# Kernel tuning notes

Measured on AMD Instinct MI355X. Metric: run time of the kernel, lower is better.

Reference implementation:

```python
import jax, jax.numpy as jnp
import numpy as np

GROUPS = 32
EPS = 1e-5
N_HEADS = 4


def group_norm(x, w, b):
    # x: [B, C, T]; GroupNorm over (C/G, T) within each of G groups
    B, C, T = x.shape
    xg = x.reshape(B, GROUPS, (C // GROUPS) * T)
    mean = xg.mean(axis=-1, keepdims=True)
    var = xg.var(axis=-1, keepdims=True)
    xn = ((xg - mean) * jax.lax.rsqrt(var + EPS)).reshape(B, C, T)
    return xn * w[None, :, None] + b[None, :, None]


def setup_inputs() -> dict:
    key = jax.random.key(0)
    ks = jax.random.split(key, 5)
    B, C, H, W = 2, 256, 64, 64
    x = jax.random.normal(ks[0], (B, C, H, W), dtype=jnp.float32)
    norm_w = jnp.ones((C,), dtype=jnp.float32)
    norm_b = jnp.zeros((C,), dtype=jnp.float32)
    qkv_w = jax.random.normal(ks[1], (3 * C, C), dtype=jnp.float32) * (C ** -0.5)
    qkv_b = jax.random.normal(ks[2], (3 * C,), dtype=jnp.float32) * 0.02
    proj_w = jax.random.normal(ks[3], (C, C), dtype=jnp.float32) * (C ** -0.5)
    proj_b = jax.random.normal(ks[4], (C,), dtype=jnp.float32) * 0.02
    return {"x": x, "norm_w": norm_w, "norm_b": norm_b,
            "qkv_w": qkv_w, "qkv_b": qkv_b,
            "proj_w": proj_w, "proj_b": proj_b}


def reference(x, norm_w, norm_b, qkv_w, qkv_b, proj_w, proj_b):
    B, C, Hs, Ws = x.shape
    T = Hs * Ws
    xf = x.reshape(B, C, T)
    xn = group_norm(xf, norm_w, norm_b)
    # 1x1 conv1d == channel matmul: [3C,C] x [B,C,T] -> [B,3C,T]
    qkv = jnp.einsum('oc,bct->bot', qkv_w, xn) + qkv_b[None, :, None]
    ch = C // N_HEADS
    # legacy order: [B, H*3*ch, T] -> [B*H, 3*ch, T] -> split
    qkv_h = qkv.reshape(B * N_HEADS, 3 * ch, T)
    q, k, v = qkv_h[:, :ch], qkv_h[:, ch:2 * ch], qkv_h[:, 2 * ch:]
    scale = ch ** -0.25
    # full [B*H, T, T] score matrix, softmax in fp32 (faithful to source)
    weight = jnp.einsum('bct,bcs->bts', q * scale, k * scale)
    weight = jax.nn.softmax(weight.astype(jnp.float32), axis=-1).astype(qkv.dtype)
    a = jnp.einsum('bts,bcs->bct', weight, v).reshape(B, C, T)
    h = jnp.einsum('oc,bct->bot', proj_w, a) + proj_b[None, :, None]
    return (xf + h).reshape(B, C, Hs, Ws)
```

## Files before the change

### kernel.cpp

```cpp
#include <hip/hip_runtime.h>
#include <hip/hip_bf16.h>

#define B_    2
#define C_    256
#define T_    4096
#define GRP   32
#define CPG   8
#define NH    4
#define CH    64
#define K3C   768
#define SPLIT 4
#define GSL   8
#define LOG2E 1.4426950408889634f

typedef __attribute__((ext_vector_type(8))) short bf16x8;
typedef __attribute__((ext_vector_type(4))) float f32x4;

#if __has_builtin(__builtin_amdgcn_exp2f)
#define EXP2(x) __builtin_amdgcn_exp2f(x)
#else
#define EXP2(x) exp2f(x)
#endif

__device__ __forceinline__ unsigned pk2(float a, float b) {
    __hip_bfloat162 h = __float22bfloat162_rn(make_float2(a, b));
    union { __hip_bfloat162 h2; unsigned u; } cv; cv.h2 = h;
    return cv.u;
}
__device__ __forceinline__ float bf2f(unsigned short u) {
    return __uint_as_float((unsigned)u << 16);
}

__global__ __launch_bounds__(256) void cvt_kernel(
    const float* __restrict__ qw, const float* __restrict__ pw,
    unsigned short* __restrict__ qwb, unsigned short* __restrict__ pwb) {
    int i = blockIdx.x * 256 + threadIdx.x;
    const int n1 = K3C * C_ / 8;
    const float* src; unsigned short* dst;
    if (i < n1) { src = qw + 8 * i; dst = qwb + 8 * i; }
    else { int j = i - n1; src = pw + 8 * j; dst = pwb + 8 * j; }
    float4 a = *(const float4*)src;
    float4 b = *(const float4*)(src + 4);
    uint4 u;
    u.x = pk2(a.x, a.y); u.y = pk2(a.z, a.w);
    u.z = pk2(b.x, b.y); u.w = pk2(b.z, b.w);
    *(uint4*)dst = u;
}

__global__ __launch_bounds__(256) void gn_stats_kernel(
    const float* __restrict__ x, float* __restrict__ stat) {
    int bg = blockIdx.x, sl = blockIdx.y;
    const int SLN = CPG * T_ / GSL;
    const float* xp = x + (size_t)bg * CPG * T_ + (size_t)sl * SLN;
    int tid = threadIdx.x;

    float s = 0.f, s2 = 0.f;
    for (int i = tid * 4; i < SLN; i += 1024) {
        float4 v = *(const float4*)&xp[i];
        s  += (v.x + v.y) + (v.z + v.w);
        s2 += (v.x * v.x + v.y * v.y) + (v.z * v.z + v.w * v.w);
    }
    for (int off = 32; off > 0; off >>= 1) {
        s  += __shfl_down(s,  off);
        s2 += __shfl_down(s2, off);
    }
    __shared__ float rs[4], rs2[4];
    int wid = tid >> 6;
    if ((tid & 63) == 0) { rs[wid] = s; rs2[wid] = s2; }
    __syncthreads();
    if (tid == 0) {
        float a = (rs[0] + rs[1]) + (rs[2] + rs[3]);
        float a2 = (rs2[0] + rs2[1]) + (rs2[2] + rs2[3]);
        stat[(bg * GSL + sl) * 2]     = a;
        stat[(bg * GSL + sl) * 2 + 1] = a2;
    }
}

__global__ __launch_bounds__(256) void gn_apply_kernel(
    const float* __restrict__ x, const float* __restrict__ stat,
    const float* __restrict__ w, const float* __restrict__ b,
    unsigned short* __restrict__ xnT) {
    int bg = blockIdx.x, sl = blockIdx.y;
    int batch = bg / GRP, g = bg % GRP;
    const float* xp = x + (size_t)bg * CPG * T_;
    int tid = threadIdx.x;

    float s = 0.f, s2 = 0.f;
#pragma unroll
    for (int i = 0; i < GSL; ++i) {
        s  += stat[(bg * GSL + i) * 2];
        s2 += stat[(bg * GSL + i) * 2 + 1];
    }
    float inv_n = 1.f / (float)(CPG * T_);
    float mean = s * inv_n;
    float var  = s2 * inv_n - mean * mean;
    float inv  = rsqrtf(var + 1e-5f);

    float wv[8], bv[8];
#pragma unroll
    for (int j = 0; j < 8; j++) {
        float ww = w[g * CPG + j] * inv;
        wv[j] = ww;
        bv[j] = b[g * CPG + j] - mean * ww;
    }
    unsigned short* op = xnT + (size_t)batch * T_ * C_ + g * CPG;
    int t0 = sl * (T_ / GSL);
#pragma unroll
    for (int rep = 0; rep < 2; ++rep) {
        int t = t0 + rep * 256 + tid;
        float v[8];
#pragma unroll
        for (int j = 0; j < 8; j++) v[j] = xp[(size_t)j * T_ + t] * wv[j] + bv[j];
        uint4 u;
        u.x = pk2(v[0], v[1]); u.y = pk2(v[2], v[3]);
        u.z = pk2(v[4], v[5]); u.w = pk2(v[6], v[7]);
        *(uint4*)&op[(size_t)t * C_] = u;
    }
}

__global__ __launch_bounds__(256) void qkv_gemm_kernel(
    const unsigned short* __restrict__ Wb, const float* __restrict__ bias,
    const unsigned short* __restrict__ Xt, unsigned short* __restrict__ q_t,
    unsigned short* __restrict__ k_t, unsigned short* __restrict__ v_d) {
    int tb = blockIdx.x * 128;
    int by = blockIdx.y;
    int bz = blockIdx.z;
    int ob = by * 64;
    int tid = threadIdx.x;
    int l = tid & 15, oct = (tid >> 4) & 3, w = tid >> 6;

    __shared__ __align__(16) unsigned short SH[64 * 264];

#pragma unroll
    for (int j = 0; j < 8; ++j) {
        int idx = tid + 256 * j;
        int row = idx >> 5, ch = idx & 31;
        *(uint4*)&SH[row * 264 + ch * 8] =
            *(const uint4*)&Wb[(size_t)(ob + row) * C_ + ch * 8];
    }
    __syncthreads();

    const unsigned short* Xb = Xt + (size_t)bz * T_ * C_;

    f32x4 acc[4][2];
#pragma unroll
    for (int mf = 0; mf < 4; ++mf)
#pragma unroll
        for (int nf = 0; nf < 2; ++nf) acc[mf][nf] = (f32x4){0.f, 0.f, 0.f, 0.f};

#pragma unroll
    for (int kk = 0; kk < 8; ++kk) {
        int c0 = 32 * kk + 8 * oct;
        bf16x8 bfr[2];
#pragma unroll
        for (int nf = 0; nf < 2; ++nf)
            bfr[nf] = *(const bf16x8*)&Xb[(size_t)(tb + 32 * w + 16 * nf + l) * C_ + c0];
#pragma unroll
        for (int mf = 0; mf < 4; ++mf) {
            bf16x8 af = *(const bf16x8*)&SH[(16 * mf + l) * 264 + c0];
#pragma unroll
            for (int nf = 0; nf < 2; ++nf)
                acc[mf][nf] = __builtin_amdgcn_mfma_f32_16x16x32_bf16(af, bfr[nf], acc[mf][nf], 0, 0, 0);
        }
    }

    int head = by / 3, sec = by - 3 * head;
    int bh = bz * NH + head;

    if (sec < 2) {
        float scale = (sec == 0) ? 0.125f * LOG2E : 1.f;
        unsigned short* dst = ((sec == 0) ? q_t : k_t) + (size_t)bh * T_ * CH;
#pragma unroll
        for (int mf = 0; mf < 4; ++mf) {
            float bvs[4];
#pragma unroll
            for (int r = 0; r < 4; ++r) bvs[r] = bias[ob + 16 * mf + 4 * oct + r];
#pragma unroll
            for (int nf = 0; nf < 2; ++nf) {
                int t = tb + 32 * w + 16 * nf + l;
                float v0 = (acc[mf][nf][0] + bvs[0]) * scale;
                float v1 = (acc[mf][nf][1] + bvs[1]) * scale;
                float v2 = (acc[mf][nf][2] + bvs[2]) * scale;
                float v3 = (acc[mf][nf][3] + bvs[3]) * scale;
                uint2 u; u.x = pk2(v0, v1); u.y = pk2(v2, v3);
                *(uint2*)&dst[(size_t)t * CH + 16 * mf + 4 * oct] = u;
            }
        }
    } else {
        __syncthreads();
#pragma unroll
        for (int mf = 0; mf < 4; ++mf) {
            float bvs[4];
#pragma unroll
            for (int r = 0; r < 4; ++r) bvs[r] = bias[ob + 16 * mf + 4 * oct + r];
#pragma unroll
            for (int nf = 0; nf < 2; ++nf) {
                int tl = 32 * w + 16 * nf + l;
#pragma unroll
                for (int r = 0; r < 4; ++r) {
                    unsigned pv = pk2(acc[mf][nf][r] + bvs[r], 0.f);
                    SH[(16 * mf + 4 * oct + r) * 136 + tl] = (unsigned short)(pv & 0xffffu);
                }
            }
        }
        __syncthreads();
        unsigned short* vdst = v_d + (size_t)bh * CH * T_;
#pragma unroll
        for (int j = 0; j < 4; ++j) {
            int idx = tid + 256 * j;
            int row = idx >> 4, ch = idx & 15;
            *(uint4*)&vdst[(size_t)row * T_ + tb + ch * 8] =
                *(uint4*)&SH[row * 136 + ch * 8];
        }
    }
}

__global__ __launch_bounds__(256, 4) void attn_kernel(
    const unsigned short* __restrict__ q_t, const unsigned short* __restrict__ k_t,
    const unsigned short* __restrict__ v_d, unsigned short* __restrict__ Opart,
    float* __restrict__ lbuf) {
    int bh = blockIdx.y;
    int sp = blockIdx.z;
    int t0 = blockIdx.x * 128;
    int tid = threadIdx.x;
    int l = tid & 15, q = (tid >> 4) & 3, w = tid >> 6;

    __shared__ __align__(16) unsigned short Kt[64][72];
    __shared__ __align__(16) unsigned short Vt[64][72];
    __shared__ __align__(16) unsigned short Ps[128][72];

    const unsigned short* qb = q_t + (size_t)bh * T_ * CH;
    const unsigned short* kb = k_t + (size_t)bh * T_ * CH;
    const unsigned short* vb = v_d + (size_t)bh * CH * T_;

    bf16x8 qf[2][2];
#pragma unroll
    for (int nf = 0; nf < 2; ++nf) {
        int t = t0 + 32 * w + 16 * nf + l;
#pragma unroll
        for (int kk = 0; kk < 2; ++kk)
            qf[nf][kk] = *(const bf16x8*)&qb[(size_t)t * CH + 32 * kk + 8 * q];
    }

    f32x4 O[4][2];
#pragma unroll
    for (int mf = 0; mf < 4; ++mf)
#pragma unroll
        for (int nf = 0; nf < 2; ++nf) O[mf][nf] = (f32x4){0.f, 0.f, 0.f, 0.f};
    float l_run[2] = {0.f, 0.f};

    int s_beg = sp * (T_ / SPLIT);
    int s_end = s_beg + (T_ / SPLIT);
    for (int s0 = s_beg; s0 < s_end; s0 += 64) {
#pragma unroll
        for (int it = 0; it < 2; ++it) {
            int row = (tid >> 3) + 32 * it;
            int ch  = tid & 7;
            *(uint4*)&Kt[row][ch * 8] =
                *(const uint4*)&kb[(size_t)(s0 + row) * CH + ch * 8];
            *(uint4*)&Vt[row][ch * 8] =
                *(const uint4*)&vb[(size_t)row * T_ + s0 + ch * 8];
        }
        __syncthreads();

        f32x4 S[4][2];
#pragma unroll
        for (int sf = 0; sf < 4; ++sf) {
            f32x4 a0 = (f32x4){0.f, 0.f, 0.f, 0.f};
            f32x4 a1 = (f32x4){0.f, 0.f, 0.f, 0.f};
#pragma unroll
            for (int kk = 0; kk < 2; ++kk) {
                bf16x8 ka = *(const bf16x8*)&Kt[16 * sf + l][32 * kk + 8 * q];
                a0 = __builtin_amdgcn_mfma_f32_16x16x32_bf16(ka, qf[0][kk], a0, 0, 0, 0);
                a1 = __builtin_amdgcn_mfma_f32_16x16x32_bf16(ka, qf[1][kk], a1, 0, 0, 0);
            }
            S[sf][0] = a0; S[sf][1] = a1;
        }

#pragma unroll
        for (int nf = 0; nf < 2; ++nf) {
            int trow = 32 * w + 16 * nf + l;
            float lloc = 0.f;
#pragma unroll
            for (int sf = 0; sf < 4; ++sf) {
                float p0 = EXP2(S[sf][nf][0]);
                float p1 = EXP2(S[sf][nf][1]);
                float p2 = EXP2(S[sf][nf][2]);
                float p3 = EXP2(S[sf][nf][3]);
                lloc += (p0 + p1) + (p2 + p3);
                uint2 u; u.x = pk2(p0, p1); u.y = pk2(p2, p3);
                *(uint2*)&Ps[trow][16 * sf + 4 * q] = u;
            }
            l_run[nf] += lloc;
        }

#pragma unroll
        for (int kk = 0; kk < 2; ++kk) {
            bf16x8 pb[2];
#pragma unroll
            for (int nf = 0; nf < 2; ++nf)
                pb[nf] = *(const bf16x8*)&Ps[32 * w + 16 * nf + l][32 * kk + 8 * q];
#pragma unroll
            for (int mf = 0; mf < 4; ++mf) {
                bf16x8 va = *(const bf16x8*)&Vt[16 * mf + l][32 * kk + 8 * q];
#pragma unroll
                for (int nf = 0; nf < 2; ++nf)
                    O[mf][nf] = __builtin_amdgcn_mfma_f32_16x16x32_bf16(va, pb[nf], O[mf][nf], 0, 0, 0);
            }
        }
        __syncthreads();
    }

#pragma unroll
    for (int nf = 0; nf < 2; ++nf) {
        float lt = l_run[nf];
        lt += __shfl_xor(lt, 16);
        lt += __shfl_xor(lt, 32);
        float inv = 1.f / lt;
        int t = t0 + 32 * w + 16 * nf + l;
        size_t row = (size_t)(sp * 8 + bh) * T_ + t;
        unsigned short* op = Opart + row * CH;
#pragma unroll
        for (int mf = 0; mf < 4; ++mf) {
            uint2 u;
            u.x = pk2(O[mf][nf][0] * inv, O[mf][nf][1] * inv);
            u.y = pk2(O[mf][nf][2] * inv, O[mf][nf][3] * inv);
            *(uint2*)&op[16 * mf + 4 * q] = u;
        }
        if (q == 0) lbuf[row] = lt;
    }
}

__global__ __launch_bounds__(256) void combine_kernel(
    const unsigned short* __restrict__ Opart, const float* __restrict__ lbuf,
    unsigned short* __restrict__ a_t) {
    int bx = blockIdx.x;
    int bh = bx >> 6;
    int tblk = bx & 63;
    int tid = threadIdx.x;
    int t = tblk * 64 + (tid >> 2);
    int sub = tid & 3;

    float lw[SPLIT];
    size_t rows[SPLIT];
    float lsum = 0.f;
#pragma unroll
    for (int sp = 0; sp < SPLIT; ++sp) {
        rows[sp] = (size_t)(sp * 8 + bh) * T_ + t;
        lw[sp] = lbuf[rows[sp]];
        lsum += lw[sp];
    }
    float inv = 1.f / lsum;

    float o[16];
#pragma unroll
    for (int i = 0; i < 16; ++i) o[i] = 0.f;
#pragma unroll
    for (int sp = 0; sp < SPLIT; ++sp) {
        float s = lw[sp] * inv;
        const unsigned short* p = Opart + rows[sp] * CH + sub * 16;
        uint4 u0 = *(const uint4*)p;
        uint4 u1 = *(const uint4*)(p + 8);
        unsigned us[8] = {u0.x, u0.y, u0.z, u0.w, u1.x, u1.y, u1.z, u1.w};
#pragma unroll
        for (int j = 0; j < 8; ++j) {
            o[2 * j]     += bf2f((unsigned short)(us[j] & 0xffffu)) * s;
            o[2 * j + 1] += bf2f((unsigned short)(us[j] >> 16)) * s;
        }
    }

    int batch = bh >> 2, h = bh & 3;
    unsigned short* dst = a_t + ((size_t)batch * T_ + t) * C_ + h * CH + sub * 16;
    uint4 u0, u1;
    u0.x = pk2(o[0], o[1]);   u0.y = pk2(o[2], o[3]);
    u0.z = pk2(o[4], o[5]);   u0.w = pk2(o[6], o[7]);
    u1.x = pk2(o[8], o[9]);   u1.y = pk2(o[10], o[11]);
    u1.z = pk2(o[12], o[13]); u1.w = pk2(o[14], o[15]);
    *(uint4*)dst = u0;
    *(uint4*)(dst + 8) = u1;
}

__global__ __launch_bounds__(256) void proj_gemm_kernel(
    const unsigned short* __restrict__ Wb, const float* __restrict__ bias,
    const unsigned short* __restrict__ At, const float* __restrict__ xres,
    float* __restrict__ out) {
    int tb = blockIdx.x * 128;
    int ob = blockIdx.y * 64;
    int bz = blockIdx.z;
    int tid = threadIdx.x;
    int l = tid & 15, oct = (tid >> 4) & 3, w = tid >> 6;

    __shared__ __align__(16) unsigned short SH[64 * 264];

#pragma unroll
    for (int j = 0; j < 8; ++j) {
        int idx = tid + 256 * j;
        int row = idx >> 5, ch = idx & 31;
        *(uint4*)&SH[row * 264 + ch * 8] =
            *(const uint4*)&Wb[(size_t)(ob + row) * C_ + ch * 8];
    }
    __syncthreads();

    const unsigned short* Ab = At + (size_t)bz * T_ * C_;

    f32x4 acc[4][2];
#pragma unroll
    for (int mf = 0; mf < 4; ++mf)
#pragma unroll
        for (int nf = 0; nf < 2; ++nf) acc[mf][nf] = (f32x4){0.f, 0.f, 0.f, 0.f};

#pragma unroll
    for (int kk = 0; kk < 8; ++kk) {
        int c0 = 32 * kk + 8 * oct;
        bf16x8 bfr[2];
#pragma unroll
        for (int nf = 0; nf < 2; ++nf)
            bfr[nf] = *(const bf16x8*)&Ab[(size_t)(tb + 32 * w + 16 * nf + l) * C_ + c0];
#pragma unroll
        for (int mf = 0; mf < 4; ++mf) {
            bf16x8 af = *(const bf16x8*)&SH[(16 * mf + l) * 264 + c0];
#pragma unroll
            for (int nf = 0; nf < 2; ++nf)
                acc[mf][nf] = __builtin_amdgcn_mfma_f32_16x16x32_bf16(af, bfr[nf], acc[mf][nf], 0, 0, 0);
        }
    }

#pragma unroll
    for (int mf = 0; mf < 4; ++mf) {
#pragma unroll
        for (int nf = 0; nf < 2; ++nf) {
            int t = tb + 32 * w + 16 * nf + l;
#pragma unroll
            for (int r = 0; r < 4; ++r) {
                int o = ob + 16 * mf + 4 * oct + r;
                size_t idx = ((size_t)bz * C_ + o) * T_ + t;
                out[idx] = acc[mf][nf][r] + bias[o] + xres[idx];
            }
        }
    }
}

extern "C" void kernel_launch(void* const* d_in, const int* in_sizes, int n_in,
                              void* d_out, int out_size, void* d_ws, size_t ws_size,
                              hipStream_t stream) {
    const float* x      = (const float*)d_in[0];
    const float* norm_w = (const float*)d_in[1];
    const float* norm_b = (const float*)d_in[2];
    const float* qkv_w  = (const float*)d_in[3];
    const float* qkv_b  = (const float*)d_in[4];
    const float* proj_w = (const float*)d_in[5];
    const float* proj_b = (const float*)d_in[6];
    float* out = (float*)d_out;

    char* p = (char*)d_ws;
    unsigned short* xnT = (unsigned short*)p; p += (size_t)B_ * T_ * C_ * 2;
    unsigned short* qwb = (unsigned short*)p; p += (size_t)K3C * C_ * 2;
    unsigned short* pwb = (unsigned short*)p; p += (size_t)C_ * C_ * 2;
    unsigned short* q_t = (unsigned short*)p; p += (size_t)B_ * NH * T_ * CH * 2;
    unsigned short* k_t = (unsigned short*)p; p += (size_t)B_ * NH * T_ * CH * 2;
    unsigned short* v_d = (unsigned short*)p; p += (size_t)B_ * NH * T_ * CH * 2;
    unsigned short* Opart = (unsigned short*)p; p += (size_t)SPLIT * 8 * T_ * CH * 2;
    float* lbuf         = (float*)p;          p += (size_t)SPLIT * 8 * T_ * 4;
    unsigned short* a_t = (unsigned short*)p; p += (size_t)B_ * T_ * C_ * 2;
    float* stat         = (float*)p;          p += (size_t)B_ * GRP * GSL * 2 * 4;

    cvt_kernel<<<dim3(128), dim3(256), 0, stream>>>(qkv_w, proj_w, qwb, pwb);
    gn_stats_kernel<<<dim3(B_ * GRP, GSL), dim3(256), 0, stream>>>(x, stat);
    gn_apply_kernel<<<dim3(B_ * GRP, GSL), dim3(256), 0, stream>>>(
        x, stat, norm_w, norm_b, xnT);
    qkv_gemm_kernel<<<dim3(T_ / 128, 12, B_), dim3(256), 0, stream>>>(
        qwb, qkv_b, xnT, q_t, k_t, v_d);
    attn_kernel<<<dim3(T_ / 128, B_ * NH, SPLIT), dim3(256), 0, stream>>>(
        q_t, k_t, v_d, Opart, lbuf);
    combine_kernel<<<dim3(B_ * NH * (T_ / 64)), dim3(256), 0, stream>>>(Opart, lbuf, a_t);
    proj_gemm_kernel<<<dim3(T_ / 128, C_ / 64, B_), dim3(256), 0, stream>>>(
        pwb, proj_b, a_t, x, out);
}
```

Measured before the change: 152.5 us.

## Prefetch K/V tiles in attention, merge prep kernels, halve proj GEMM tile

The attention loop now loads the next K/V tile from global memory into registers right after the barrier. This overlaps that load latency with the current tile's MFMA and softmax work. The group-norm stats kernel and the weight conversion kernel are merged into one launch, removing a kernel launch. The projection GEMM tile is halved to 64 time steps per block, giving twice as many blocks for better CU occupancy, at the cost of more reloads of the weight tile into shared memory.

```diff
diff --git a/kernel.cpp b/kernel.cpp
--- a/kernel.cpp
+++ b/kernel.cpp
@@ -11,6 +11,8 @@
 #define K3C   768
 #define SPLIT 4
 #define GSL   8
+#define NSTAT (B_ * GRP * GSL)
+#define NCVT  128
 #define LOG2E 1.4426950408889634f
 
 typedef __attribute__((ext_vector_type(8))) short bf16x8;
@@ -31,48 +33,46 @@
     return __uint_as_float((unsigned)u << 16);
 }
 
-__global__ __launch_bounds__(256) void cvt_kernel(
+__global__ __launch_bounds__(256) void pre_kernel(
+    const float* __restrict__ x, float* __restrict__ stat,
     const float* __restrict__ qw, const float* __restrict__ pw,
     unsigned short* __restrict__ qwb, unsigned short* __restrict__ pwb) {
-    int i = blockIdx.x * 256 + threadIdx.x;
-    const int n1 = K3C * C_ / 8;
-    const float* src; unsigned short* dst;
-    if (i < n1) { src = qw + 8 * i; dst = qwb + 8 * i; }
-    else { int j = i - n1; src = pw + 8 * j; dst = pwb + 8 * j; }
-    float4 a = *(const float4*)src;
-    float4 b = *(const float4*)(src + 4);
-    uint4 u;
-    u.x = pk2(a.x, a.y); u.y = pk2(a.z, a.w);
-    u.z = pk2(b.x, b.y); u.w = pk2(b.z, b.w);
-    *(uint4*)dst = u;
-}
-
-__global__ __launch_bounds__(256) void gn_stats_kernel(
-    const float* __restrict__ x, float* __restrict__ stat) {
-    int bg = blockIdx.x, sl = blockIdx.y;
-    const int SLN = CPG * T_ / GSL;
-    const float* xp = x + (size_t)bg * CPG * T_ + (size_t)sl * SLN;
-    int tid = threadIdx.x;
-
-    float s = 0.f, s2 = 0.f;
-    for (int i = tid * 4; i < SLN; i += 1024) {
-        float4 v = *(const float4*)&xp[i];
-        s  += (v.x + v.y) + (v.z + v.w);
-        s2 += (v.x * v.x + v.y * v.y) + (v.z * v.z + v.w * v.w);
-    }
-    for (int off = 32; off > 0; off >>= 1) {
-        s  += __shfl_down(s,  off);
-        s2 += __shfl_down(s2, off);
-    }
-    __shared__ float rs[4], rs2[4];
-    int wid = tid >> 6;
-    if ((tid & 63) == 0) { rs[wid] = s; rs2[wid] = s2; }
-    __syncthreads();
-    if (tid == 0) {
-        float a = (rs[0] + rs[1]) + (rs[2] + rs[3]);
-        float a2 = (rs2[0] + rs2[1]) + (rs2[2] + rs2[3]);
-        stat[(bg * GSL + sl) * 2]     = a;
-        stat[(bg * GSL + sl) * 2 + 1] = a2;
+    int bid = blockIdx.x;
+    int tid = threadIdx.x;
+    if (bid < NSTAT) {
+        int bg = bid >> 3, sl = bid & 7;
+        const int SLN = CPG * T_ / GSL;
+        const float* xp = x + (size_t)bg * CPG * T_ + (size_t)sl * SLN;
+        float s = 0.f, s2 = 0.f;
+        for (int i = tid * 4; i < SLN; i += 1024) {
+            float4 v = *(const float4*)&xp[i];
+            s  += (v.x + v.y) + (v.z + v.w);
+            s2 += (v.x * v.x + v.y * v.y) + (v.z * v.z + v.w * v.w);
+        }
+        for (int off = 32; off > 0; off >>= 1) {
+            s  += __shfl_down(s,  off);
+            s2 += __shfl_down(s2, off);
+        }
+        __shared__ float rs[4], rs2[4];
+        int wid = tid >> 6;
+        if ((tid & 63) == 0) { rs[wid] = s; rs2[wid] = s2; }
+        __syncthreads();
+        if (tid == 0) {
+            stat[bid * 2]     = (rs[0] + rs[1]) + (rs[2] + rs[3]);
+            stat[bid * 2 + 1] = (rs2[0] + rs2[1]) + (rs2[2] + rs2[3]);
+        }
+    } else {
+        int i = (bid - NSTAT) * 256 + tid;
+        const int n1 = K3C * C_ / 8;
+        const float* src; unsigned short* dst;
+        if (i < n1) { src = qw + 8 * i; dst = qwb + 8 * i; }
+        else { int j = i - n1; src = pw + 8 * j; dst = pwb + 8 * j; }
+        float4 a = *(const float4*)src;
+        float4 b = *(const float4*)(src + 4);
+        uint4 u;
+        u.x = pk2(a.x, a.y); u.y = pk2(a.z, a.w);
+        u.z = pk2(b.x, b.y); u.w = pk2(b.z, b.w);
+        *(uint4*)dst = u;
     }
 }
 
@@ -242,6 +242,13 @@
             qf[nf][kk] = *(const bf16x8*)&qb[(size_t)t * CH + 32 * kk + 8 * q];
     }
 
+    int srow = tid >> 3;
+    int sch8 = (tid & 7) * 8;
+    const unsigned short* kp0 = kb + (size_t)srow * CH + sch8;
+    const unsigned short* kp1 = kb + (size_t)(srow + 32) * CH + sch8;
+    const unsigned short* vp0 = vb + (size_t)srow * T_ + sch8;
+    const unsigned short* vp1 = vb + (size_t)(srow + 32) * T_ + sch8;
+
     f32x4 O[4][2];
 #pragma unroll
     for (int mf = 0; mf < 4; ++mf)
@@ -251,17 +258,26 @@
 
     int s_beg = sp * (T_ / SPLIT);
     int s_end = s_beg + (T_ / SPLIT);
+
+    uint4 kreg0 = *(const uint4*)(kp0 + (size_t)s_beg * CH);
+    uint4 kreg1 = *(const uint4*)(kp1 + (size_t)s_beg * CH);
+    uint4 vreg0 = *(const uint4*)(vp0 + s_beg);
+    uint4 vreg1 = *(const uint4*)(vp1 + s_beg);
+
     for (int s0 = s_beg; s0 < s_end; s0 += 64) {
-#pragma unroll
-        for (int it = 0; it < 2; ++it) {
-            int row = (tid >> 3) + 32 * it;
-            int ch  = tid & 7;
-            *(uint4*)&Kt[row][ch * 8] =
-                *(const uint4*)&kb[(size_t)(s0 + row) * CH + ch * 8];
-            *(uint4*)&Vt[row][ch * 8] =
-                *(const uint4*)&vb[(size_t)row * T_ + s0 + ch * 8];
-        }
+        *(uint4*)&Kt[srow][sch8]      = kreg0;
+        *(uint4*)&Kt[srow + 32][sch8] = kreg1;
+        *(uint4*)&Vt[srow][sch8]      = vreg0;
+        *(uint4*)&Vt[srow + 32][sch8] = vreg1;
         __syncthreads();
+
+        int sn = s0 + 64;
+        if (sn < s_end) {
+            kreg0 = *(const uint4*)(kp0 + (size_t)sn * CH);
+            kreg1 = *(const uint4*)(kp1 + (size_t)sn * CH);
+            vreg0 = *(const uint4*)(vp0 + sn);
+            vreg1 = *(const uint4*)(vp1 + sn);
+        }
 
         f32x4 S[4][2];
 #pragma unroll
@@ -384,7 +400,7 @@
     const unsigned short* __restrict__ Wb, const float* __restrict__ bias,
     const unsigned short* __restrict__ At, const float* __restrict__ xres,
     float* __restrict__ out) {
-    int tb = blockIdx.x * 128;
+    int tb = blockIdx.x * 64;
     int ob = blockIdx.y * 64;
     int bz = blockIdx.z;
     int tid = threadIdx.x;
@@ -402,40 +418,30 @@
     __syncthreads();
 
     const unsigned short* Ab = At + (size_t)bz * T_ * C_;
-
-    f32x4 acc[4][2];
-#pragma unroll
-    for (int mf = 0; mf < 4; ++mf)
-#pragma unroll
-        for (int nf = 0; nf < 2; ++nf) acc[mf][nf] = (f32x4){0.f, 0.f, 0.f, 0.f};
+    int t = tb + 16 * w + l;
+
+    f32x4 acc[4];
+#pragma unroll
+    for (int mf = 0; mf < 4; ++mf) acc[mf] = (f32x4){0.f, 0.f, 0.f, 0.f};
 
 #pragma unroll
     for (int kk = 0; kk < 8; ++kk) {
         int c0 = 32 * kk + 8 * oct;
-        bf16x8 bfr[2];
-#pragma unroll
-        for (int nf = 0; nf < 2; ++nf)
-            bfr[nf] = *(const bf16x8*)&Ab[(size_t)(tb + 32 * w + 16 * nf + l) * C_ + c0];
+        bf16x8 bfr = *(const bf16x8*)&Ab[(size_t)t * C_ + c0];
 #pragma unroll
         for (int mf = 0; mf < 4; ++mf) {
             bf16x8 af = *(const bf16x8*)&SH[(16 * mf + l) * 264 + c0];
-#pragma unroll
-            for (int nf = 0; nf < 2; ++nf)
-                acc[mf][nf] = __builtin_amdgcn_mfma_f32_16x16x32_bf16(af, bfr[nf], acc[mf][nf], 0, 0, 0);
+            acc[mf] = __builtin_amdgcn_mfma_f32_16x16x32_bf16(af, bfr, acc[mf], 0, 0, 0);
         }
     }
 
 #pragma unroll
     for (int mf = 0; mf < 4; ++mf) {
 #pragma unroll
-        for (int nf = 0; nf < 2; ++nf) {
-            int t = tb + 32 * w + 16 * nf + l;
-#pragma unroll
-            for (int r = 0; r < 4; ++r) {
-                int o = ob + 16 * mf + 4 * oct + r;
-                size_t idx = ((size_t)bz * C_ + o) * T_ + t;
-                out[idx] = acc[mf][nf][r] + bias[o] + xres[idx];
-            }
+        for (int r = 0; r < 4; ++r) {
+            int o = ob + 16 * mf + 4 * oct + r;
+            size_t idx = ((size_t)bz * C_ + o) * T_ + t;
+            out[idx] = acc[mf][r] + bias[o] + xres[idx];
         }
     }
 }
@@ -462,10 +468,10 @@
     unsigned short* Opart = (unsigned short*)p; p += (size_t)SPLIT * 8 * T_ * CH * 2;
     float* lbuf         = (float*)p;          p += (size_t)SPLIT * 8 * T_ * 4;
     unsigned short* a_t = (unsigned short*)p; p += (size_t)B_ * T_ * C_ * 2;
-    float* stat         = (float*)p;          p += (size_t)B_ * GRP * GSL * 2 * 4;
-
-    cvt_kernel<<<dim3(128), dim3(256), 0, stream>>>(qkv_w, proj_w, qwb, pwb);
-    gn_stats_kernel<<<dim3(B_ * GRP, GSL), dim3(256), 0, stream>>>(x, stat);
+    float* stat         = (float*)p;          p += (size_t)NSTAT * 2 * 4;
+
+    pre_kernel<<<dim3(NSTAT + NCVT), dim3(256), 0, stream>>>(
+        x, stat, qkv_w, proj_w, qwb, pwb);
     gn_apply_kernel<<<dim3(B_ * GRP, GSL), dim3(256), 0, stream>>>(
         x, stat, norm_w, norm_b, xnT);
     qkv_gemm_kernel<<<dim3(T_ / 128, 12, B_), dim3(256), 0, stream>>>(
@@ -473,6 +479,6 @@
     attn_kernel<<<dim3(T_ / 128, B_ * NH, SPLIT), dim3(256), 0, stream>>>(
         q_t, k_t, v_d, Opart, lbuf);
     combine_kernel<<<dim3(B_ * NH * (T_ / 64)), dim3(256), 0, stream>>>(Opart, lbuf, a_t);
-    proj_gemm_kernel<<<dim3(T_ / 128, C_ / 64, B_), dim3(256), 0, stream>>>(
+    proj_gemm_kernel<<<dim3(T_ / 64, C_ / 64, B_), dim3(256), 0, stream>>>(
         pwb, proj_b, a_t, x, out);
 }
```

Result: faster. 149.5 us (-2.0%).
